# Performance work log

Measured on AMD Instinct MI355X. Metric: run time of the kernel, lower is better.

Reference implementation:

```python
import jax, jax.numpy as jnp
import numpy as np

EPS = 1e-5  # BatchNorm1d default eps


def _xavier_uniform(key, shape):
    # torch xavier: fan_in = shape[1]*prod(shape[2:]), fan_out = shape[0]*prod(shape[2:])
    rf = int(np.prod(shape[2:])) if len(shape) > 2 else 1
    fan_in = shape[1] * rf
    fan_out = shape[0] * rf
    bound = float(np.sqrt(6.0 / (fan_in + fan_out)))
    return jax.random.uniform(key, shape, jnp.float32, -bound, bound)


def setup_inputs() -> dict:
    key = jax.random.key(0)
    ks = jax.random.split(key, 6)
    d_in, h1, h2, d_out = 256, 512, 512, 256
    B = 4096
    x = jax.random.normal(ks[0], (B, 1, d_in), dtype=jnp.float32)
    W1 = _xavier_uniform(ks[1], (h1, d_in))
    b1 = jnp.zeros((h1,), jnp.float32)
    gamma = jnp.ones((1, 1, 1), jnp.float32)   # BatchNorm1d(1) weight
    beta = jnp.zeros((1, 1, 1), jnp.float32)   # BatchNorm1d(1) bias
    coeffs2 = _xavier_uniform(ks[2], (2, h2, h1, 16))
    bias2 = jnp.zeros((1, h2), jnp.float32)
    coeffs3 = _xavier_uniform(ks[3], (2, d_out, h2, 8))
    bias3 = jnp.zeros((1, d_out), jnp.float32)
    return {"x": x, "W1": W1, "b1": b1, "gamma": gamma, "beta": beta,
            "coeffs2": coeffs2, "bias2": bias2, "coeffs3": coeffs3, "bias3": bias3}


def _fourier_kan(x, coeffs, bias, gridsize):
    # x: (N, in)  coeffs: (2, out, in, grid)  ->  (N, out)
    k = jnp.arange(1, gridsize + 1, dtype=x.dtype)          # (grid,)
    arg = x[:, :, None] * k                                  # (N, in, grid) -- basis computed ONCE
    y = jnp.einsum('nig,oig->no', jnp.cos(arg), coeffs[0])
    y = y + jnp.einsum('nig,oig->no', jnp.sin(arg), coeffs[1])
    return y + bias


def reference(x, W1, b1, gamma, beta, coeffs2, bias2, coeffs3, bias3):
    # x: (B, 1, d_in)
    h = jnp.einsum('bcd,hd->bch', x, W1) + b1                # Linear -> (B,1,h1)
    # BatchNorm1d(1), training-mode batch stats over (N, L) for the single channel
    mean = jnp.mean(h, axis=(0, 2), keepdims=True)
    var = jnp.mean((h - mean) ** 2, axis=(0, 2), keepdims=True)
    h = gamma * (h - mean) * jax.lax.rsqrt(var + EPS) + beta
    h = jax.nn.relu(h)
    h = h.reshape(-1, h.shape[-1])                           # (B, h1)
    h = _fourier_kan(h, coeffs2, bias2, 16)                  # (B, h2)
    h = _fourier_kan(h, coeffs3, bias3, 8)                   # (B, out)
    return jax.nn.softmax(h, axis=1)
```

## Files before the change

kernel.cpp:

```cpp
#include <hip/hip_runtime.h>
#include <hip/hip_fp16.h>
#include <stdint.h>

typedef unsigned short u16;
typedef unsigned int u32;
typedef long i64;
typedef short bf16x8 __attribute__((ext_vector_type(8)));
typedef float f32x4 __attribute__((ext_vector_type(4)));

#define SCALE_C   1024.f
#define INV_SCALE 0.0009765625f

__device__ __forceinline__ float bf2f(u16 v) { return __uint_as_float(((u32)v) << 16); }

__device__ __forceinline__ u16 f2bf(float a) {
  u32 u = __float_as_uint(a); u += 0x7FFFu + ((u >> 16) & 1u); return (u16)(u >> 16);
}

__device__ __forceinline__ u32 packbf2(float a, float b) {
  u32 ua = __float_as_uint(a); ua += 0x7FFFu + ((ua >> 16) & 1u);
  u32 ub = __float_as_uint(b); ub += 0x7FFFu + ((ub >> 16) & 1u);
  return (ua >> 16) | (ub & 0xFFFF0000u);
}

__device__ __forceinline__ u32 packfp8x4(float a, float b, float c, float d) {
  u32 lo = (u32)__builtin_amdgcn_cvt_pk_fp8_f32(a, b, 0, false);
  return (u32)__builtin_amdgcn_cvt_pk_fp8_f32(c, d, (int)lo, true);
}

__device__ __forceinline__ float inval(const void* p, int idx, int isf) {
  return isf ? ((const float*)p)[idx] : bf2f(((const u16*)p)[idx]);
}

__device__ __forceinline__ void async_cp16(const void* g, void* l) {
  __builtin_amdgcn_global_load_lds(
      (const __attribute__((address_space(1))) void*)g,
      (__attribute__((address_space(3))) void*)l, 16, 0, 0);
}

__device__ __forceinline__ void basis16(float a, u32* pk) {
  float s1, c1; __sincosf(a, &s1, &c1);
  float t2 = c1 + c1;
  float cg[16], sg[16];
  cg[0] = c1; sg[0] = s1;
  cg[1] = fmaf(t2, c1, -1.f); sg[1] = t2 * s1;
  #pragma unroll
  for (int g = 2; g < 16; ++g) {
    cg[g] = fmaf(t2, cg[g-1], -cg[g-2]);
    sg[g] = fmaf(t2, sg[g-1], -sg[g-2]);
  }
  #pragma unroll
  for (int j = 0; j < 4; ++j) pk[j]   = packfp8x4(cg[4*j], cg[4*j+1], cg[4*j+2], cg[4*j+3]);
  #pragma unroll
  for (int j = 0; j < 4; ++j) pk[4+j] = packfp8x4(sg[4*j], sg[4*j+1], sg[4*j+2], sg[4*j+3]);
}

__device__ __forceinline__ void basis8(float a, u32* pk) {
  float s1, c1; __sincosf(a, &s1, &c1);
  float t2 = c1 + c1;
  float cg[8], sg[8];
  cg[0] = c1; sg[0] = s1;
  cg[1] = fmaf(t2, c1, -1.f); sg[1] = t2 * s1;
  #pragma unroll
  for (int g = 2; g < 8; ++g) {
    cg[g] = fmaf(t2, cg[g-1], -cg[g-2]);
    sg[g] = fmaf(t2, sg[g-1], -sg[g-2]);
  }
  pk[0] = packfp8x4(cg[0], cg[1], cg[2], cg[3]);
  pk[1] = packfp8x4(cg[4], cg[5], cg[6], cg[7]);
  pk[2] = packfp8x4(sg[0], sg[1], sg[2], sg[3]);
  pk[3] = packfp8x4(sg[4], sg[5], sg[6], sg[7]);
}

#define QOF(k) ((size_t)((k) < 6 ? (k) * 4 : 26 + ((k) - 6) * 4) << 20)

__device__ __forceinline__ void split_body(
    const void* __restrict__ src, u16* __restrict__ dst, int i, int isf, int lo_pos)
{
  int row = i >> 6, g = i & 63;
  float v[4];
  if (isf) {
    float4 t = ((const float4*)src)[i];
    v[0] = t.x; v[1] = t.y; v[2] = t.z; v[3] = t.w;
  } else {
    uint2 t = ((const uint2*)src)[i];
    const u16* p = (const u16*)&t;
    v[0] = bf2f(p[0]); v[1] = bf2f(p[1]); v[2] = bf2f(p[2]); v[3] = bf2f(p[3]);
  }
  u16 hi[4]; float lo[4];
  #pragma unroll
  for (int j = 0; j < 4; ++j) { hi[j] = f2bf(v[j]); lo[j] = v[j] - bf2f(hi[j]); }
  u32 hw0 = (u32)hi[0] | ((u32)hi[1] << 16);
  u32 hw1 = (u32)hi[2] | ((u32)hi[3] << 16);
  u32 lw0 = packbf2(lo[0], lo[1]);
  u32 lw1 = packbf2(lo[2], lo[3]);
  u32* base = (u32*)(dst + (size_t)row * 768);
  int c = g * 2;
  base[c] = hw0; base[c + 1] = hw1;
  if (lo_pos == 1) {
    base[128 + c] = lw0; base[128 + c + 1] = lw1;
    base[256 + c] = hw0; base[256 + c + 1] = hw1;
  } else {
    base[128 + c] = hw0; base[128 + c + 1] = hw1;
    base[256 + c] = lw0; base[256 + c + 1] = lw1;
  }
}

__global__ __launch_bounds__(256) void prep_all_kernel(
    const void* __restrict__ x, const void* __restrict__ W1,
    u16* __restrict__ Xs, u16* __restrict__ W1s,
    const void* __restrict__ c2, unsigned char* __restrict__ w2f8,
    const void* __restrict__ c3, unsigned char* __restrict__ w3f8,
    int* __restrict__ flag)
{
  __shared__ int sf[4];
  const int t = threadIdx.x, wave = t >> 6;
  {
    float v = fabsf(bf2f(((const u16*)W1)[t & 127]));
    int bad = !(v < 1e6f);
    unsigned long long b = __ballot(bad);
    if ((t & 63) == 0) sf[wave] = (b != 0ull) ? 1 : 0;
  }
  __syncthreads();
  const int isf = sf[0] | sf[1] | sf[2] | sf[3];
  const int bid = blockIdx.x;
  if (bid == 0 && t == 0) *flag = isf;
  if (bid < 1024) {
    split_body(x, Xs, bid * 256 + t, isf, 1);
  } else if (bid < 1152) {
    split_body(W1, W1s, (bid - 1024) * 256 + t, isf, 2);
  } else if (bid < 2176) {
    int u = (bid - 1152) * 256 + t;
    int o = u >> 9, i = u & 511;
    u32* d = (u32*)(w2f8 + (size_t)o * 16384 + i * 32);
    if (isf) {
      const float4* f0 = (const float4*)((const float*)c2 + ((size_t)o * 512 + i) * 16);
      const float4* f1 = (const float4*)((const float*)c2 + (size_t)512 * 512 * 16 + ((size_t)o * 512 + i) * 16);
      #pragma unroll
      for (int j = 0; j < 4; ++j) { float4 v = f0[j]; d[j]   = packfp8x4(v.x*SCALE_C, v.y*SCALE_C, v.z*SCALE_C, v.w*SCALE_C); }
      #pragma unroll
      for (int j = 0; j < 4; ++j) { float4 v = f1[j]; d[4+j] = packfp8x4(v.x*SCALE_C, v.y*SCALE_C, v.z*SCALE_C, v.w*SCALE_C); }
    } else {
      const u16* s0 = (const u16*)c2 + ((size_t)o * 512 + i) * 16;
      const u16* s1 = (const u16*)c2 + (size_t)512 * 512 * 16 + ((size_t)o * 512 + i) * 16;
      #pragma unroll
      for (int j = 0; j < 4; ++j) d[j]   = packfp8x4(bf2f(s0[4*j])*SCALE_C, bf2f(s0[4*j+1])*SCALE_C, bf2f(s0[4*j+2])*SCALE_C, bf2f(s0[4*j+3])*SCALE_C);
      #pragma unroll
      for (int j = 0; j < 4; ++j) d[4+j] = packfp8x4(bf2f(s1[4*j])*SCALE_C, bf2f(s1[4*j+1])*SCALE_C, bf2f(s1[4*j+2])*SCALE_C, bf2f(s1[4*j+3])*SCALE_C);
    }
  } else {
    int u = (bid - 2176) * 256 + t;
    int o = u >> 9, i = u & 511;
    u32* d = (u32*)(w3f8 + (size_t)o * 8192 + i * 16);
    if (isf) {
      const float4* f0 = (const float4*)((const float*)c3 + ((size_t)o * 512 + i) * 8);
      const float4* f1 = (const float4*)((const float*)c3 + (size_t)256 * 512 * 8 + ((size_t)o * 512 + i) * 8);
      #pragma unroll
      for (int j = 0; j < 2; ++j) { float4 v = f0[j]; d[j]   = packfp8x4(v.x*SCALE_C, v.y*SCALE_C, v.z*SCALE_C, v.w*SCALE_C); }
      #pragma unroll
      for (int j = 0; j < 2; ++j) { float4 v = f1[j]; d[2+j] = packfp8x4(v.x*SCALE_C, v.y*SCALE_C, v.z*SCALE_C, v.w*SCALE_C); }
    } else {
      const u16* s0 = (const u16*)c3 + ((size_t)o * 512 + i) * 8;
      const u16* s1 = (const u16*)c3 + (size_t)256 * 512 * 8 + ((size_t)o * 512 + i) * 8;
      #pragma unroll
      for (int j = 0; j < 2; ++j) d[j]   = packfp8x4(bf2f(s0[4*j])*SCALE_C, bf2f(s0[4*j+1])*SCALE_C, bf2f(s0[4*j+2])*SCALE_C, bf2f(s0[4*j+3])*SCALE_C);
      #pragma unroll
      for (int j = 0; j < 2; ++j) d[2+j] = packfp8x4(bf2f(s1[4*j])*SCALE_C, bf2f(s1[4*j+1])*SCALE_C, bf2f(s1[4*j+2])*SCALE_C, bf2f(s1[4*j+3])*SCALE_C);
    }
  }
}

#define L1_LD 136
__global__ __launch_bounds__(256) void l1_kernel(
    const u16* __restrict__ xs, const u16* __restrict__ w1s, const void* __restrict__ b1,
    const int* __restrict__ flag, float* __restrict__ H, float2* __restrict__ PT)
{
  __shared__ u16 sA[64 * L1_LD];
  __shared__ u16 sB[64 * L1_LD];
  __shared__ float redbuf[8];
  const int n0 = blockIdx.x * 64, o0 = blockIdx.y * 64;
  const int t = threadIdx.x, wave = t >> 6, lane = t & 63, quad = lane >> 4, l16 = lane & 15;
  const int isf = *flag;
  f32x4 acc[4] = {};
  for (int ks = 0; ks < 768; ks += 128) {
    #pragma unroll
    for (int r = 0; r < 4; ++r) {
      int idx = t + r * 256, row = idx >> 4, col = idx & 15;
      *(uint4*)&sA[row * L1_LD + col * 8] =
          *((const uint4*)(xs + (size_t)(n0 + row) * 768 + ks) + col);
    }
    #pragma unroll
    for (int r = 0; r < 4; ++r) {
      int idx = t + r * 256, row = idx >> 4, col = idx & 15;
      *(uint4*)&sB[row * L1_LD + col * 8] =
          *((const uint4*)(w1s + (size_t)(o0 + row) * 768 + ks) + col);
    }
    __syncthreads();
    #pragma unroll
    for (int kk = 0; kk < 128; kk += 32) {
      bf16x8 av = *(const bf16x8*)&sA[(wave * 16 + l16) * L1_LD + kk + quad * 8];
      #pragma unroll
      for (int fo = 0; fo < 4; ++fo) {
        bf16x8 bv = *(const bf16x8*)&sB[(fo * 16 + l16) * L1_LD + kk + quad * 8];
        acc[fo] = __builtin_amdgcn_mfma_f32_16x16x32_bf16(av, bv, acc[fo], 0, 0, 0);
      }
    }
    __syncthreads();
  }
  float s = 0.f, sq = 0.f;
  #pragma unroll
  for (int fo = 0; fo < 4; ++fo) {
    int o = o0 + fo * 16 + l16;
    float bias = inval(b1, o, isf);
    #pragma unroll
    for (int r = 0; r < 4; ++r) {
      int n = n0 + wave * 16 + quad * 4 + r;
      float h = acc[fo][r] + bias;
      H[(size_t)n * 512 + o] = h;
      s += h; sq += h * h;
    }
  }
  #pragma unroll
  for (int off = 32; off; off >>= 1) { s += __shfl_down(s, off); sq += __shfl_down(sq, off); }
  if (lane == 0) { redbuf[wave] = s; redbuf[4 + wave] = sq; }
  __syncthreads();
  if (t == 0) {
    float S = redbuf[0] + redbuf[1] + redbuf[2] + redbuf[3];
    float Q = redbuf[4] + redbuf[5] + redbuf[6] + redbuf[7];
    PT[blockIdx.y * 64 + blockIdx.x] = make_float2(S, Q);
  }
}

#define K2_LDB 128
__global__ __launch_bounds__(512, 4) void kan2_kernel(
    const float* __restrict__ H, const unsigned char* __restrict__ w2f8,
    const void* __restrict__ gammap, const void* __restrict__ betap,
    const int* __restrict__ flag, const float2* __restrict__ PT,
    float* __restrict__ P, int kzT)
{
  __shared__ __attribute__((aligned(16))) unsigned char smem[81920];
  float* sred = (float*)(smem + 81888);
  const int n0 = blockIdx.x * 64, o0 = blockIdx.y * 256, kz = blockIdx.z;
  const int t = threadIdx.x, wave = t >> 6, lane = t & 63, quad = lane >> 4, l16 = lane & 15;
  const int nst = 128 / kzT;
  const int i0 = kz * nst * 4;
  const int csw = (l16 & 7) << 4;
  const int isf = *flag;

  const int pt = t - 256;
  const int am = pt >> 2, ai = pt & 3;
  const int r0 = pt >> 3, seg = pt & 7;
  const unsigned char* bsrc = w2f8 + (size_t)(o0 + (r0 & 63)) * 16384 + (size_t)i0 * 32
                              + (((seg & 7) * 16) ^ ((r0 & 7) << 4));
  const float* hsrc = H + (size_t)(n0 + (am & 63)) * 512 + i0 + (ai & 3);
  const int acol0 = ((ai & 3) * 32) ^ ((am & 7) << 4);
  const int acol1 = ((ai & 3) * 32 + 16) ^ ((am & 7) << 4);
  float mean = 0.f, gs = 0.f, beta = 0.f, ph = 0.f;
  u32 pk[8];

  if (wave >= 4) {
    unsigned char* b0 = smem + 16384 + (wave - 4) * 1024;
    #pragma unroll
    for (int p = 0; p < 8; ++p)
      async_cp16(bsrc + (size_t)p * 32 * 16384, b0 + p * 4096);
    float2 pa = PT[pt], pb = PT[pt + 256];
    float ss = pa.x + pb.x, qs = pa.y + pb.y;
    #pragma unroll
    for (int off = 32; off; off >>= 1) { ss += __shfl_down(ss, off); qs += __shfl_down(qs, off); }
    if (lane == 0) { sred[(wave - 4) * 2] = ss; sred[(wave - 4) * 2 + 1] = qs; }
  }
  __syncthreads();
  if (wave >= 4) {
    const float Ssum = sred[0] + sred[2] + sred[4] + sred[6];
    const float Qsum = sred[1] + sred[3] + sred[5] + sred[7];
    const float Nn = 4096.f * 512.f;
    mean = Ssum / Nn;
    const float rstd = rsqrtf(Qsum / Nn - mean * mean + 1e-5f);
    gs = inval(gammap, 0, isf) * rstd;
    beta = inval(betap, 0, isf);
    float a = fmaxf((*hsrc - mean) * gs + beta, 0.f);
    hsrc += 4;
    basis16(a, pk);
    *(uint4*)&smem[am * K2_LDB + acol0] = *(uint4*)&pk[0];
    *(uint4*)&smem[am * K2_LDB + acol1] = *(uint4*)&pk[4];
    if (nst > 1) { ph = *hsrc; hsrc += 4; }
  }
  __syncthreads();

  f32x4 acc[2][8] = {};
  const int wm = (wave & 1) * 32, wo = (wave >> 1) * 128;
  int cur = 0;
  for (int s = 0; s < nst; ++s) {
    const int nxt = cur ^ 1;
    if (wave >= 4) {
      if (s + 1 < nst) {
        bsrc += 128;
        unsigned char* bn = smem + 16384 + nxt * 32768 + (wave - 4) * 1024;
        #pragma unroll
        for (int p = 0; p < 8; ++p)
          async_cp16(bsrc + (size_t)p * 32 * 16384, bn + p * 4096);
        float a = fmaxf((ph - mean) * gs + beta, 0.f);
        basis16(a, pk);
        unsigned char* an = smem + nxt * 8192;
        *(uint4*)&an[am * K2_LDB + acol0] = *(uint4*)&pk[0];
        *(uint4*)&an[am * K2_LDB + acol1] = *(uint4*)&pk[4];
        if (s + 2 < nst) { ph = *hsrc; hsrc += 4; }
      }
    } else {
      const unsigned char* ac = smem + cur * 8192;
      const unsigned char* bc = smem + 16384 + cur * 32768;
      #pragma unroll
      for (int kk = 0; kk < 128; kk += 32) {
        const int cb = (kk + quad * 8) ^ csw;
        i64 bfr[8], afr[2];
        #pragma unroll
        for (int fo = 0; fo < 8; ++fo)
          bfr[fo] = *(const i64*)&bc[(wo + fo * 16 + l16) * K2_LDB + cb];
        #pragma unroll
        for (int fm = 0; fm < 2; ++fm)
          afr[fm] = *(const i64*)&ac[(wm + fm * 16 + l16) * K2_LDB + cb];
        #pragma unroll
        for (int fm = 0; fm < 2; ++fm)
        #pragma unroll
        for (int fo = 0; fo < 8; ++fo)
          acc[fm][fo] = __builtin_amdgcn_mfma_f32_16x16x32_fp8_fp8(afr[fm], bfr[fo], acc[fm][fo], 0, 0, 0);
      }
    }
    __syncthreads();
    cur = nxt;
  }
  if (wave < 4) {
    float* Pk = P + (size_t)kz * (4096 * 512);
    #pragma unroll
    for (int fm = 0; fm < 2; ++fm)
    #pragma unroll
    for (int fo = 0; fo < 8; ++fo) {
      int o = o0 + wo + fo * 16 + l16;
      #pragma unroll
      for (int r = 0; r < 4; ++r) {
        int n = n0 + wm + fm * 16 + quad * 4 + r;
        Pk[(size_t)n * 512 + o] = acc[fm][fo][r] * INV_SCALE;
      }
    }
  }
}

#define K3_LDB 128
__global__ __launch_bounds__(512, 4) void kan3_kernel(
    const float* __restrict__ P2, const void* __restrict__ bias2,
    const unsigned char* __restrict__ w3f8,
    const int* __restrict__ flag, char* __restrict__ wsbase, int kzT2)
{
  __shared__ __attribute__((aligned(16))) unsigned char smem[81920];
  const int n0 = blockIdx.x * 64, kz = blockIdx.z;
  const int t = threadIdx.x, wave = t >> 6, lane = t & 63, quad = lane >> 4, l16 = lane & 15;
  const int i0 = kz * 64;
  const int nst = 8;
  const int csw = (l16 & 7) << 4;
  const int isf = *flag;

  const int pt = t - 256;
  const int am = (pt >> 2) & 63;
  const int il = (pt & 3) * 2;
  const int r0 = (pt >> 3) & 31, seg = pt & 7;
  const unsigned char* bsrc = w3f8 + (size_t)r0 * 8192 + (size_t)i0 * 16
                              + ((seg * 16) ^ ((r0 & 7) << 4));
  const float* psrc = P2 + (size_t)(n0 + am) * 512 + i0 + il;
  const int acol0 = (il * 16) ^ ((am & 7) << 4);
  const int acol1 = ((il + 1) * 16) ^ ((am & 7) << 4);
  float2 ph2 = make_float2(0.f, 0.f);
  u32 pkA[4], pkB[4];

  if (wave >= 4) {
    unsigned char* b0 = smem + 16384 + (wave - 4) * 1024;
    #pragma unroll
    for (int p = 0; p < 8; ++p)
      async_cp16(bsrc + (size_t)p * 32 * 8192, b0 + p * 4096);
    float v0 = inval(bias2, i0 + il, isf);
    float v1 = inval(bias2, i0 + il + 1, isf);
    for (int k = 0; k < kzT2; ++k) {
      float2 pp = *(const float2*)(psrc + (size_t)k * 4096 * 512);
      v0 += pp.x; v1 += pp.y;
    }
    basis8(v0, pkA); basis8(v1, pkB);
    *(uint4*)&smem[am * K3_LDB + acol0] = *(uint4*)&pkA[0];
    *(uint4*)&smem[am * K3_LDB + acol1] = *(uint4*)&pkB[0];
    psrc += 8;
    float w0 = inval(bias2, i0 + 8 + il, isf);
    float w1 = inval(bias2, i0 + 8 + il + 1, isf);
    for (int k = 0; k < kzT2; ++k) {
      float2 pp = *(const float2*)(psrc + (size_t)k * 4096 * 512);
      w0 += pp.x; w1 += pp.y;
    }
    ph2 = make_float2(w0, w1);
  }
  __syncthreads();

  f32x4 acc[4][4] = {};
  const int wo = wave * 64;
  int cur = 0;
  for (int s = 0; s < nst; ++s) {
    const int nxt = cur ^ 1;
    if (wave >= 4) {
      if (s + 1 < nst) {
        bsrc += 128;
        unsigned char* bn = smem + 16384 + nxt * 32768 + (wave - 4) * 1024;
        #pragma unroll
        for (int p = 0; p < 8; ++p)
          async_cp16(bsrc + (size_t)p * 32 * 8192, bn + p * 4096);
        basis8(ph2.x, pkA); basis8(ph2.y, pkB);
        unsigned char* an = smem + nxt * 8192;
        *(uint4*)&an[am * K3_LDB + acol0] = *(uint4*)&pkA[0];
        *(uint4*)&an[am * K3_LDB + acol1] = *(uint4*)&pkB[0];
        if (s + 2 < nst) {
          psrc += 8;
          float w0 = inval(bias2, i0 + (s + 2) * 8 + il, isf);
          float w1 = inval(bias2, i0 + (s + 2) * 8 + il + 1, isf);
          for (int k = 0; k < kzT2; ++k) {
            float2 pp = *(const float2*)(psrc + (size_t)k * 4096 * 512);
            w0 += pp.x; w1 += pp.y;
          }
          ph2 = make_float2(w0, w1);
        }
      }
    } else {
      const unsigned char* ac = smem + cur * 8192;
      const unsigned char* bc = smem + 16384 + cur * 32768;
      __builtin_amdgcn_s_setprio(1);
      #pragma unroll
      for (int kk = 0; kk < 128; kk += 32) {
        const int cb = (kk + quad * 8) ^ csw;
        i64 bfr[4], afr[4];
        #pragma unroll
        for (int fo = 0; fo < 4; ++fo)
          bfr[fo] = *(const i64*)&bc[(wo + fo * 16 + l16) * K3_LDB + cb];
        #pragma unroll
        for (int fm = 0; fm < 4; ++fm)
          afr[fm] = *(const i64*)&ac[(fm * 16 + l16) * K3_LDB + cb];
        #pragma unroll
        for (int fm = 0; fm < 4; ++fm)
        #pragma unroll
        for (int fo = 0; fo < 4; ++fo)
          acc[fm][fo] = __builtin_amdgcn_mfma_f32_16x16x32_fp8_fp8(afr[fm], bfr[fo], acc[fm][fo], 0, 0, 0);
      }
      __builtin_amdgcn_s_setprio(0);
    }
    __syncthreads();
    cur = nxt;
  }
  if (wave < 4) {
    float* Qk = (float*)(wsbase + QOF(kz));
    #pragma unroll
    for (int fm = 0; fm < 4; ++fm)
    #pragma unroll
    for (int fo = 0; fo < 4; ++fo) {
      int o = wo + fo * 16 + l16;
      #pragma unroll
      for (int r = 0; r < 4; ++r) {
        int n = n0 + fm * 16 + quad * 4 + r;
        Qk[(size_t)n * 256 + o] = acc[fm][fo][r] * INV_SCALE;
      }
    }
  }
}

__global__ __launch_bounds__(256) void softmax_kernel(
    const char* __restrict__ wsbase, const void* __restrict__ bias3,
    const int* __restrict__ flag, float* __restrict__ out)
{
  const int t = threadIdx.x, wave = t >> 6, lane = t & 63;
  const int row = blockIdx.x * 4 + wave;
  const int isf = *flag;
  size_t base = (size_t)row * 256 + lane * 4;
  float v0 = 0.f, v1 = 0.f, v2 = 0.f, v3 = 0.f;
  #pragma unroll
  for (int k = 0; k < 8; ++k) {
    float4 a = *(const float4*)((const float*)(wsbase + QOF(k)) + base);
    v0 += a.x; v1 += a.y; v2 += a.z; v3 += a.w;
  }
  int o = lane * 4;
  v0 += inval(bias3, o + 0, isf);
  v1 += inval(bias3, o + 1, isf);
  v2 += inval(bias3, o + 2, isf);
  v3 += inval(bias3, o + 3, isf);
  float m = fmaxf(fmaxf(v0, v1), fmaxf(v2, v3));
  #pragma unroll
  for (int off = 32; off; off >>= 1) m = fmaxf(m, __shfl_xor(m, off));
  float e0 = __expf(v0 - m), e1 = __expf(v1 - m), e2 = __expf(v2 - m), e3 = __expf(v3 - m);
  float s = e0 + e1 + e2 + e3;
  #pragma unroll
  for (int off = 32; off; off >>= 1) s += __shfl_xor(s, off);
  float inv = 1.f / s;
  *(float4*)(out + base) = make_float4(e0 * inv, e1 * inv, e2 * inv, e3 * inv);
}

extern "C" void kernel_launch(void* const* d_in, const int* in_sizes, int n_in,
                              void* d_out, int out_size, void* d_ws, size_t ws_size,
                              hipStream_t stream)
{
  const void* x     = d_in[0];
  const void* W1    = d_in[1];
  const void* b1    = d_in[2];
  const void* gamma = d_in[3];
  const void* beta  = d_in[4];
  const void* c2    = d_in[5];
  const void* bias2 = d_in[6];
  const void* c3    = d_in[7];
  const void* bias3 = d_in[8];

  const int kz2 = 4;

  char* ws = (char*)d_ws;
  float*          H    = (float*)(ws + 0);
  unsigned char*  W2F8 = (unsigned char*)(ws + (16ull << 20));
  unsigned char*  W3F8 = (unsigned char*)(ws + (24ull << 20));
  u16*            Xs   = (u16*)(ws + (26ull << 20));
  u16*            W1s  = (u16*)(ws + (33ull << 20));
  float*          P2   = (float*)(ws + (34ull << 20));
  size_t tail = (34ull << 20) + (size_t)kz2 * (8ull << 20) + 524288;
  float2* PT   = (float2*)(ws + tail);
  int*    FLAG = (int*)   (ws + tail + 65536);

  prep_all_kernel<<<dim3(2688), dim3(256), 0, stream>>>(x, W1, Xs, W1s, c2, W2F8, c3, W3F8, FLAG);
  l1_kernel   <<<dim3(64, 8), dim3(256), 0, stream>>>(Xs, W1s, b1, FLAG, H, PT);
  kan2_kernel <<<dim3(64, 2, kz2), dim3(512), 0, stream>>>(H, W2F8, gamma, beta, FLAG, PT, P2, kz2);
  kan3_kernel <<<dim3(64, 1, 8), dim3(512), 0, stream>>>(P2, bias2, W3F8, FLAG, ws, kz2);
  softmax_kernel<<<dim3(1024), dim3(256), 0, stream>>>(ws, bias3, FLAG, (float*)d_out);
}
```

Baseline: 195.2 us.

## Replace split-K partial buffers with atomic accumulation into zeroed buffers

Split-K partial sums in the two KAN layers are now accumulated with float atomics into one buffer per layer, instead of being written as separate slices and summed by the consumer kernels. The prep kernel gets extra blocks that zero the accumulation buffers (12MB). This cuts the consumer-side reads of 4 or 8 partial slices and shrinks the workspace footprint. In exchange it adds atomic traffic and a zeroing pass, and makes the summation order nondeterministic.

```diff
diff --git a/kernel.cpp b/kernel.cpp
--- a/kernel.cpp
+++ b/kernel.cpp
@@ -36,6 +36,10 @@
   __builtin_amdgcn_global_load_lds(
       (const __attribute__((address_space(1))) void*)g,
       (__attribute__((address_space(3))) void*)l, 16, 0, 0);
+}
+
+__device__ __forceinline__ void atomic_fadd(float* p, float v) {
+  (void)unsafeAtomicAdd(p, v);
 }
 
 __device__ __forceinline__ void basis16(float a, u32* pk) {
@@ -71,8 +75,6 @@
   pk[2] = packfp8x4(sg[0], sg[1], sg[2], sg[3]);
   pk[3] = packfp8x4(sg[4], sg[5], sg[6], sg[7]);
 }
-
-#define QOF(k) ((size_t)((k) < 6 ? (k) * 4 : 26 + ((k) - 6) * 4) << 20)
 
 __device__ __forceinline__ void split_body(
     const void* __restrict__ src, u16* __restrict__ dst, int i, int isf, int lo_pos)
@@ -111,10 +113,18 @@
     u16* __restrict__ Xs, u16* __restrict__ W1s,
     const void* __restrict__ c2, unsigned char* __restrict__ w2f8,
     const void* __restrict__ c3, unsigned char* __restrict__ w3f8,
-    int* __restrict__ flag)
+    int* __restrict__ flag, unsigned char* __restrict__ zero_base)
 {
   __shared__ int sf[4];
   const int t = threadIdx.x, wave = t >> 6;
+  const int bid = blockIdx.x;
+  if (bid >= 2688) {
+    uint4* dst = (uint4*)(zero_base + (size_t)(bid - 2688) * 65536);
+    uint4 z = make_uint4(0, 0, 0, 0);
+    #pragma unroll
+    for (int j = 0; j < 16; ++j) dst[j * 256 + t] = z;
+    return;
+  }
   {
     float v = fabsf(bf2f(((const u16*)W1)[t & 127]));
     int bad = !(v < 1e6f);
@@ -123,7 +133,6 @@
   }
   __syncthreads();
   const int isf = sf[0] | sf[1] | sf[2] | sf[3];
-  const int bid = blockIdx.x;
   if (bid == 0 && t == 0) *flag = isf;
   if (bid < 1024) {
     split_body(x, Xs, bid * 256 + t, isf, 1);
@@ -330,7 +339,6 @@
     cur = nxt;
   }
   if (wave < 4) {
-    float* Pk = P + (size_t)kz * (4096 * 512);
     #pragma unroll
     for (int fm = 0; fm < 2; ++fm)
     #pragma unroll
@@ -339,7 +347,7 @@
       #pragma unroll
       for (int r = 0; r < 4; ++r) {
         int n = n0 + wm + fm * 16 + quad * 4 + r;
-        Pk[(size_t)n * 512 + o] = acc[fm][fo][r] * INV_SCALE;
+        atomic_fadd(&P[(size_t)n * 512 + o], acc[fm][fo][r] * INV_SCALE);
       }
     }
   }
@@ -349,7 +357,7 @@
 __global__ __launch_bounds__(512, 4) void kan3_kernel(
     const float* __restrict__ P2, const void* __restrict__ bias2,
     const unsigned char* __restrict__ w3f8,
-    const int* __restrict__ flag, char* __restrict__ wsbase, int kzT2)
+    const int* __restrict__ flag, float* __restrict__ Q3)
 {
   __shared__ __attribute__((aligned(16))) unsigned char smem[81920];
   const int n0 = blockIdx.x * 64, kz = blockIdx.z;
@@ -376,23 +384,16 @@
     #pragma unroll
     for (int p = 0; p < 8; ++p)
       async_cp16(bsrc + (size_t)p * 32 * 8192, b0 + p * 4096);
-    float v0 = inval(bias2, i0 + il, isf);
-    float v1 = inval(bias2, i0 + il + 1, isf);
-    for (int k = 0; k < kzT2; ++k) {
-      float2 pp = *(const float2*)(psrc + (size_t)k * 4096 * 512);
-      v0 += pp.x; v1 += pp.y;
-    }
+    float2 pp = *(const float2*)psrc;
+    float v0 = inval(bias2, i0 + il, isf) + pp.x;
+    float v1 = inval(bias2, i0 + il + 1, isf) + pp.y;
     basis8(v0, pkA); basis8(v1, pkB);
     *(uint4*)&smem[am * K3_LDB + acol0] = *(uint4*)&pkA[0];
     *(uint4*)&smem[am * K3_LDB + acol1] = *(uint4*)&pkB[0];
     psrc += 8;
-    float w0 = inval(bias2, i0 + 8 + il, isf);
-    float w1 = inval(bias2, i0 + 8 + il + 1, isf);
-    for (int k = 0; k < kzT2; ++k) {
-      float2 pp = *(const float2*)(psrc + (size_t)k * 4096 * 512);
-      w0 += pp.x; w1 += pp.y;
-    }
-    ph2 = make_float2(w0, w1);
+    float2 pq = *(const float2*)psrc;
+    ph2 = make_float2(inval(bias2, i0 + 8 + il, isf) + pq.x,
+                      inval(bias2, i0 + 8 + il + 1, isf) + pq.y);
   }
   __syncthreads();
 
@@ -414,13 +415,9 @@
         *(uint4*)&an[am * K3_LDB + acol1] = *(uint4*)&pkB[0];
         if (s + 2 < nst) {
           psrc += 8;
-          float w0 = inval(bias2, i0 + (s + 2) * 8 + il, isf);
-          float w1 = inval(bias2, i0 + (s + 2) * 8 + il + 1, isf);
-          for (int k = 0; k < kzT2; ++k) {
-            float2 pp = *(const float2*)(psrc + (size_t)k * 4096 * 512);
-            w0 += pp.x; w1 += pp.y;
-          }
-          ph2 = make_float2(w0, w1);
+          float2 pq = *(const float2*)psrc;
+          ph2 = make_float2(inval(bias2, i0 + (s + 2) * 8 + il, isf) + pq.x,
+                            inval(bias2, i0 + (s + 2) * 8 + il + 1, isf) + pq.y);
         }
       }
     } else {
@@ -449,7 +446,6 @@
     cur = nxt;
   }
   if (wave < 4) {
-    float* Qk = (float*)(wsbase + QOF(kz));
     #pragma unroll
     for (int fm = 0; fm < 4; ++fm)
     #pragma unroll
@@ -458,31 +454,26 @@
       #pragma unroll
       for (int r = 0; r < 4; ++r) {
         int n = n0 + fm * 16 + quad * 4 + r;
-        Qk[(size_t)n * 256 + o] = acc[fm][fo][r] * INV_SCALE;
+        atomic_fadd(&Q3[(size_t)n * 256 + o], acc[fm][fo][r] * INV_SCALE);
       }
     }
   }
 }
 
 __global__ __launch_bounds__(256) void softmax_kernel(
-    const char* __restrict__ wsbase, const void* __restrict__ bias3,
+    const float* __restrict__ Q, const void* __restrict__ bias3,
     const int* __restrict__ flag, float* __restrict__ out)
 {
   const int t = threadIdx.x, wave = t >> 6, lane = t & 63;
   const int row = blockIdx.x * 4 + wave;
   const int isf = *flag;
   size_t base = (size_t)row * 256 + lane * 4;
-  float v0 = 0.f, v1 = 0.f, v2 = 0.f, v3 = 0.f;
-  #pragma unroll
-  for (int k = 0; k < 8; ++k) {
-    float4 a = *(const float4*)((const float*)(wsbase + QOF(k)) + base);
-    v0 += a.x; v1 += a.y; v2 += a.z; v3 += a.w;
-  }
+  float4 a = *(const float4*)(Q + base);
   int o = lane * 4;
-  v0 += inval(bias3, o + 0, isf);
-  v1 += inval(bias3, o + 1, isf);
-  v2 += inval(bias3, o + 2, isf);
-  v3 += inval(bias3, o + 3, isf);
+  float v0 = a.x + inval(bias3, o + 0, isf);
+  float v1 = a.y + inval(bias3, o + 1, isf);
+  float v2 = a.z + inval(bias3, o + 2, isf);
+  float v3 = a.w + inval(bias3, o + 3, isf);
   float m = fmaxf(fmaxf(v0, v1), fmaxf(v2, v3));
   #pragma unroll
   for (int off = 32; off; off >>= 1) m = fmaxf(m, __shfl_xor(m, off));
@@ -511,19 +502,20 @@
   const int kz2 = 4;
 
   char* ws = (char*)d_ws;
-  float*          H    = (float*)(ws + 0);
-  unsigned char*  W2F8 = (unsigned char*)(ws + (16ull << 20));
-  unsigned char*  W3F8 = (unsigned char*)(ws + (24ull << 20));
-  u16*            Xs   = (u16*)(ws + (26ull << 20));
-  u16*            W1s  = (u16*)(ws + (33ull << 20));
-  float*          P2   = (float*)(ws + (34ull << 20));
-  size_t tail = (34ull << 20) + (size_t)kz2 * (8ull << 20) + 524288;
-  float2* PT   = (float2*)(ws + tail);
-  int*    FLAG = (int*)   (ws + tail + 65536);
-
-  prep_all_kernel<<<dim3(2688), dim3(256), 0, stream>>>(x, W1, Xs, W1s, c2, W2F8, c3, W3F8, FLAG);
+  float*          H     = (float*)(ws + 0);
+  unsigned char*  W2F8  = (unsigned char*)(ws + (16ull << 20));
+  unsigned char*  W3F8  = (unsigned char*)(ws + (24ull << 20));
+  u16*            Xs    = (u16*)(ws + (26ull << 20));
+  u16*            W1s   = (u16*)(ws + (33ull << 20));
+  float*          P2ACC = (float*)(ws + (34ull << 20));
+  float*          Q3ACC = (float*)(ws + (42ull << 20));
+  float2*         PT    = (float2*)(ws + (47ull << 20));
+  int*            FLAG  = (int*)  (ws + (47ull << 20) + 65536);
+  unsigned char*  ZBASE = (unsigned char*)(ws + (34ull << 20));
+
+  prep_all_kernel<<<dim3(2880), dim3(256), 0, stream>>>(x, W1, Xs, W1s, c2, W2F8, c3, W3F8, FLAG, ZBASE);
   l1_kernel   <<<dim3(64, 8), dim3(256), 0, stream>>>(Xs, W1s, b1, FLAG, H, PT);
-  kan2_kernel <<<dim3(64, 2, kz2), dim3(512), 0, stream>>>(H, W2F8, gamma, beta, FLAG, PT, P2, kz2);
-  kan3_kernel <<<dim3(64, 1, 8), dim3(512), 0, stream>>>(P2, bias2, W3F8, FLAG, ws, kz2);
-  softmax_kernel<<<dim3(1024), dim3(256), 0, stream>>>(ws, bias3, FLAG, (float*)d_out);
-}
+  kan2_kernel <<<dim3(64, 2, kz2), dim3(512), 0, stream>>>(H, W2F8, gamma, beta, FLAG, PT, P2ACC, kz2);
+  kan3_kernel <<<dim3(64, 1, 8), dim3(512), 0, stream>>>(P2ACC, bias2, W3F8, FLAG, Q3ACC);
+  softmax_kernel<<<dim3(1024), dim3(256), 0, stream>>>(Q3ACC, bias3, FLAG, (float*)d_out);
+}
```

Result: slower. 245.0 us (+25.5%).

## Drop split-K in kan3, tile over rows and outputs with full-K loop

Applied to the files above, without the earlier changes.

Replaces kan3's 8-way split-K grid (64x1x8, 64 rows by 256 outputs per block) with a 128x2 grid of 32 rows by 128 outputs, each block looping over the full K in 32 stages. This removes the eight partial-sum buffers and the 8-way reduction in softmax, which now reads a single Q3 buffer. The cost is fewer MFMAs per shared-memory A load and more serial stages per block. Each block still recomputes the fourier basis for its rows across the whole input dimension, doubled across the two output tiles.

```diff
diff --git a/kernel.cpp b/kernel.cpp
--- a/kernel.cpp
+++ b/kernel.cpp
@@ -71,8 +71,6 @@
   pk[2] = packfp8x4(sg[0], sg[1], sg[2], sg[3]);
   pk[3] = packfp8x4(sg[4], sg[5], sg[6], sg[7]);
 }
-
-#define QOF(k) ((size_t)((k) < 6 ? (k) * 4 : 26 + ((k) - 6) * 4) << 20)
 
 __device__ __forceinline__ void split_body(
     const void* __restrict__ src, u16* __restrict__ dst, int i, int isf, int lo_pos)
@@ -345,49 +343,49 @@
   }
 }
 
-#define K3_LDB 128
+#define K3_ROW 256
 __global__ __launch_bounds__(512, 4) void kan3_kernel(
     const float* __restrict__ P2, const void* __restrict__ bias2,
     const unsigned char* __restrict__ w3f8,
-    const int* __restrict__ flag, char* __restrict__ wsbase, int kzT2)
+    const int* __restrict__ flag, float* __restrict__ Q3, int kzT2)
 {
   __shared__ __attribute__((aligned(16))) unsigned char smem[81920];
-  const int n0 = blockIdx.x * 64, kz = blockIdx.z;
+  const int n0 = blockIdx.x * 32, o0 = blockIdx.y * 128;
   const int t = threadIdx.x, wave = t >> 6, lane = t & 63, quad = lane >> 4, l16 = lane & 15;
-  const int i0 = kz * 64;
-  const int nst = 8;
+  const int nst = 32;
   const int csw = (l16 & 7) << 4;
   const int isf = *flag;
 
   const int pt = t - 256;
-  const int am = (pt >> 2) & 63;
-  const int il = (pt & 3) * 2;
-  const int r0 = (pt >> 3) & 31, seg = pt & 7;
-  const unsigned char* bsrc = w3f8 + (size_t)r0 * 8192 + (size_t)i0 * 16
-                              + ((seg * 16) ^ ((r0 & 7) << 4));
-  const float* psrc = P2 + (size_t)(n0 + am) * 512 + i0 + il;
+  const int am = (pt >> 3) & 31;
+  const int il = (pt & 7) * 2;
+  const int brow0 = ((pt >> 6) & 3) * 4 + ((pt & 63) >> 4);
+  const int bcol = (pt & 15) * 16;
+  const int scol = bcol ^ ((brow0 & 7) << 4);
+  const unsigned char* bsrc = w3f8 + (size_t)(o0 + brow0) * 8192 + scol;
+  const float* psrc = P2 + (size_t)(n0 + am) * 512 + il;
   const int acol0 = (il * 16) ^ ((am & 7) << 4);
   const int acol1 = ((il + 1) * 16) ^ ((am & 7) << 4);
   float2 ph2 = make_float2(0.f, 0.f);
   u32 pkA[4], pkB[4];
 
   if (wave >= 4) {
-    unsigned char* b0 = smem + 16384 + (wave - 4) * 1024;
-    #pragma unroll
-    for (int p = 0; p < 8; ++p)
-      async_cp16(bsrc + (size_t)p * 32 * 8192, b0 + p * 4096);
-    float v0 = inval(bias2, i0 + il, isf);
-    float v1 = inval(bias2, i0 + il + 1, isf);
+    unsigned char* b0 = smem + 16384 + (pt >> 6) * 1024;
+    #pragma unroll
+    for (int q = 0; q < 8; ++q)
+      async_cp16(bsrc + (size_t)q * 16 * 8192, b0 + q * 4096);
+    float v0 = inval(bias2, il, isf);
+    float v1 = inval(bias2, il + 1, isf);
     for (int k = 0; k < kzT2; ++k) {
       float2 pp = *(const float2*)(psrc + (size_t)k * 4096 * 512);
       v0 += pp.x; v1 += pp.y;
     }
     basis8(v0, pkA); basis8(v1, pkB);
-    *(uint4*)&smem[am * K3_LDB + acol0] = *(uint4*)&pkA[0];
-    *(uint4*)&smem[am * K3_LDB + acol1] = *(uint4*)&pkB[0];
-    psrc += 8;
-    float w0 = inval(bias2, i0 + 8 + il, isf);
-    float w1 = inval(bias2, i0 + 8 + il + 1, isf);
+    *(uint4*)&smem[am * K3_ROW + acol0] = *(uint4*)&pkA[0];
+    *(uint4*)&smem[am * K3_ROW + acol1] = *(uint4*)&pkB[0];
+    psrc += 16;
+    float w0 = inval(bias2, 16 + il, isf);
+    float w1 = inval(bias2, 16 + il + 1, isf);
     for (int k = 0; k < kzT2; ++k) {
       float2 pp = *(const float2*)(psrc + (size_t)k * 4096 * 512);
       w0 += pp.x; w1 += pp.y;
@@ -396,26 +394,26 @@
   }
   __syncthreads();
 
-  f32x4 acc[4][4] = {};
-  const int wo = wave * 64;
+  f32x4 acc[4] = {};
+  const int wm = (wave & 1) * 16, wo = (wave >> 1) * 64;
   int cur = 0;
   for (int s = 0; s < nst; ++s) {
     const int nxt = cur ^ 1;
     if (wave >= 4) {
       if (s + 1 < nst) {
-        bsrc += 128;
-        unsigned char* bn = smem + 16384 + nxt * 32768 + (wave - 4) * 1024;
-        #pragma unroll
-        for (int p = 0; p < 8; ++p)
-          async_cp16(bsrc + (size_t)p * 32 * 8192, bn + p * 4096);
+        bsrc += 256;
+        unsigned char* bn = smem + 16384 + nxt * 32768 + (pt >> 6) * 1024;
+        #pragma unroll
+        for (int q = 0; q < 8; ++q)
+          async_cp16(bsrc + (size_t)q * 16 * 8192, bn + q * 4096);
         basis8(ph2.x, pkA); basis8(ph2.y, pkB);
         unsigned char* an = smem + nxt * 8192;
-        *(uint4*)&an[am * K3_LDB + acol0] = *(uint4*)&pkA[0];
-        *(uint4*)&an[am * K3_LDB + acol1] = *(uint4*)&pkB[0];
+        *(uint4*)&an[am * K3_ROW + acol0] = *(uint4*)&pkA[0];
+        *(uint4*)&an[am * K3_ROW + acol1] = *(uint4*)&pkB[0];
         if (s + 2 < nst) {
-          psrc += 8;
-          float w0 = inval(bias2, i0 + (s + 2) * 8 + il, isf);
-          float w1 = inval(bias2, i0 + (s + 2) * 8 + il + 1, isf);
+          psrc += 16;
+          float w0 = inval(bias2, (s + 2) * 16 + il, isf);
+          float w1 = inval(bias2, (s + 2) * 16 + il + 1, isf);
           for (int k = 0; k < kzT2; ++k) {
             float2 pp = *(const float2*)(psrc + (size_t)k * 4096 * 512);
             w0 += pp.x; w1 += pp.y;
@@ -428,20 +426,16 @@
       const unsigned char* bc = smem + 16384 + cur * 32768;
       __builtin_amdgcn_s_setprio(1);
       #pragma unroll
-      for (int kk = 0; kk < 128; kk += 32) {
+      for (int kk = 0; kk < 256; kk += 32) {
         const int cb = (kk + quad * 8) ^ csw;
-        i64 bfr[4], afr[4];
+        i64 bfr[4];
         #pragma unroll
         for (int fo = 0; fo < 4; ++fo)
-          bfr[fo] = *(const i64*)&bc[(wo + fo * 16 + l16) * K3_LDB + cb];
-        #pragma unroll
-        for (int fm = 0; fm < 4; ++fm)
-          afr[fm] = *(const i64*)&ac[(fm * 16 + l16) * K3_LDB + cb];
-        #pragma unroll
-        for (int fm = 0; fm < 4; ++fm)
+          bfr[fo] = *(const i64*)&bc[(wo + fo * 16 + l16) * K3_ROW + cb];
+        i64 af = *(const i64*)&ac[(wm + l16) * K3_ROW + cb];
         #pragma unroll
         for (int fo = 0; fo < 4; ++fo)
-          acc[fm][fo] = __builtin_amdgcn_mfma_f32_16x16x32_fp8_fp8(afr[fm], bfr[fo], acc[fm][fo], 0, 0, 0);
+          acc[fo] = __builtin_amdgcn_mfma_f32_16x16x32_fp8_fp8(af, bfr[fo], acc[fo], 0, 0, 0);
       }
       __builtin_amdgcn_s_setprio(0);
     }
@@ -449,40 +443,32 @@
     cur = nxt;
   }
   if (wave < 4) {
-    float* Qk = (float*)(wsbase + QOF(kz));
-    #pragma unroll
-    for (int fm = 0; fm < 4; ++fm)
     #pragma unroll
     for (int fo = 0; fo < 4; ++fo) {
-      int o = wo + fo * 16 + l16;
+      int o = o0 + wo + fo * 16 + l16;
       #pragma unroll
       for (int r = 0; r < 4; ++r) {
-        int n = n0 + fm * 16 + quad * 4 + r;
-        Qk[(size_t)n * 256 + o] = acc[fm][fo][r] * INV_SCALE;
+        int n = n0 + wm + quad * 4 + r;
+        Q3[(size_t)n * 256 + o] = acc[fo][r] * INV_SCALE;
       }
     }
   }
 }
 
 __global__ __launch_bounds__(256) void softmax_kernel(
-    const char* __restrict__ wsbase, const void* __restrict__ bias3,
+    const float* __restrict__ Q, const void* __restrict__ bias3,
     const int* __restrict__ flag, float* __restrict__ out)
 {
   const int t = threadIdx.x, wave = t >> 6, lane = t & 63;
   const int row = blockIdx.x * 4 + wave;
   const int isf = *flag;
   size_t base = (size_t)row * 256 + lane * 4;
-  float v0 = 0.f, v1 = 0.f, v2 = 0.f, v3 = 0.f;
-  #pragma unroll
-  for (int k = 0; k < 8; ++k) {
-    float4 a = *(const float4*)((const float*)(wsbase + QOF(k)) + base);
-    v0 += a.x; v1 += a.y; v2 += a.z; v3 += a.w;
-  }
+  float4 a = *(const float4*)(Q + base);
   int o = lane * 4;
-  v0 += inval(bias3, o + 0, isf);
-  v1 += inval(bias3, o + 1, isf);
-  v2 += inval(bias3, o + 2, isf);
-  v3 += inval(bias3, o + 3, isf);
+  float v0 = a.x + inval(bias3, o + 0, isf);
+  float v1 = a.y + inval(bias3, o + 1, isf);
+  float v2 = a.z + inval(bias3, o + 2, isf);
+  float v3 = a.w + inval(bias3, o + 3, isf);
   float m = fmaxf(fmaxf(v0, v1), fmaxf(v2, v3));
   #pragma unroll
   for (int off = 32; off; off >>= 1) m = fmaxf(m, __shfl_xor(m, off));
@@ -517,6 +503,7 @@
   u16*            Xs   = (u16*)(ws + (26ull << 20));
   u16*            W1s  = (u16*)(ws + (33ull << 20));
   float*          P2   = (float*)(ws + (34ull << 20));
+  float*          Q3   = (float*)(ws + 0);
   size_t tail = (34ull << 20) + (size_t)kz2 * (8ull << 20) + 524288;
   float2* PT   = (float2*)(ws + tail);
   int*    FLAG = (int*)   (ws + tail + 65536);
@@ -524,6 +511,6 @@
   prep_all_kernel<<<dim3(2688), dim3(256), 0, stream>>>(x, W1, Xs, W1s, c2, W2F8, c3, W3F8, FLAG);
   l1_kernel   <<<dim3(64, 8), dim3(256), 0, stream>>>(Xs, W1s, b1, FLAG, H, PT);
   kan2_kernel <<<dim3(64, 2, kz2), dim3(512), 0, stream>>>(H, W2F8, gamma, beta, FLAG, PT, P2, kz2);
-  kan3_kernel <<<dim3(64, 1, 8), dim3(512), 0, stream>>>(P2, bias2, W3F8, FLAG, ws, kz2);
-  softmax_kernel<<<dim3(1024), dim3(256), 0, stream>>>(ws, bias3, FLAG, (float*)d_out);
-}
+  kan3_kernel <<<dim3(128, 2), dim3(512), 0, stream>>>(P2, bias2, W3F8, FLAG, Q3, kz2);
+  softmax_kernel<<<dim3(1024), dim3(256), 0, stream>>>(Q3, bias3, FLAG, (float*)d_out);
+}
```

Measured after the change: 223.6 us. 14.6% more time.

## Double-buffer layer-1 GEMM tiles with async global-to-LDS copies and XOR swizzle

Applied to the files above, without the earlier changes.

Replaces the synchronous register-staged tile loads in l1_kernel with async 16-byte global-to-LDS copies into two 32KB buffers. The next K-slice is prefetched while the MFMAs run on the current one, leaving one barrier per step. The padded LDS layout is replaced by an XOR swizzle to avoid bank conflicts. LDS use grows to 64KB per block, which may reduce occupancy, and correctness depends on async_cp16 completing before the barrier.

```diff
diff --git a/kernel.cpp b/kernel.cpp
--- a/kernel.cpp
+++ b/kernel.cpp
@@ -170,42 +170,56 @@
   }
 }
 
-#define L1_LD 136
 __global__ __launch_bounds__(256) void l1_kernel(
     const u16* __restrict__ xs, const u16* __restrict__ w1s, const void* __restrict__ b1,
     const int* __restrict__ flag, float* __restrict__ H, float2* __restrict__ PT)
 {
-  __shared__ u16 sA[64 * L1_LD];
-  __shared__ u16 sB[64 * L1_LD];
+  __shared__ __attribute__((aligned(16))) unsigned char smem[65536];
   __shared__ float redbuf[8];
   const int n0 = blockIdx.x * 64, o0 = blockIdx.y * 64;
   const int t = threadIdx.x, wave = t >> 6, lane = t & 63, quad = lane >> 4, l16 = lane & 15;
   const int isf = *flag;
+  const int srow = lane >> 4;
+  const int scol = (lane & 15) * 16;
   f32x4 acc[4] = {};
-  for (int ks = 0; ks < 768; ks += 128) {
-    #pragma unroll
-    for (int r = 0; r < 4; ++r) {
-      int idx = t + r * 256, row = idx >> 4, col = idx & 15;
-      *(uint4*)&sA[row * L1_LD + col * 8] =
-          *((const uint4*)(xs + (size_t)(n0 + row) * 768 + ks) + col);
-    }
-    #pragma unroll
-    for (int r = 0; r < 4; ++r) {
-      int idx = t + r * 256, row = idx >> 4, col = idx & 15;
-      *(uint4*)&sB[row * L1_LD + col * 8] =
-          *((const uint4*)(w1s + (size_t)(o0 + row) * 768 + ks) + col);
-    }
+  #pragma unroll
+  for (int p = 0; p < 4; ++p) {
+    int row = (wave * 4 + p) * 4 + srow;
+    int sb = scol ^ ((row & 7) << 4);
+    async_cp16(xs  + (size_t)(n0 + row) * 768 + (sb >> 1),
+               smem + (wave * 4 + p) * 1024);
+    async_cp16(w1s + (size_t)(o0 + row) * 768 + (sb >> 1),
+               smem + 16384 + (wave * 4 + p) * 1024);
+  }
+  int cur = 0;
+  for (int s = 0; s < 6; ++s) {
     __syncthreads();
+    if (s + 1 < 6) {
+      const int ksn = (s + 1) * 128;
+      unsigned char* bufn = smem + (cur ^ 1) * 32768;
+      #pragma unroll
+      for (int p = 0; p < 4; ++p) {
+        int row = (wave * 4 + p) * 4 + srow;
+        int sb = scol ^ ((row & 7) << 4);
+        async_cp16(xs  + (size_t)(n0 + row) * 768 + ksn + (sb >> 1),
+                   bufn + (wave * 4 + p) * 1024);
+        async_cp16(w1s + (size_t)(o0 + row) * 768 + ksn + (sb >> 1),
+                   bufn + 16384 + (wave * 4 + p) * 1024);
+      }
+    }
+    const unsigned char* ba = smem + cur * 32768;
+    const unsigned char* bb = ba + 16384;
     #pragma unroll
     for (int kk = 0; kk < 128; kk += 32) {
-      bf16x8 av = *(const bf16x8*)&sA[(wave * 16 + l16) * L1_LD + kk + quad * 8];
+      const int cb = (kk * 2 + quad * 16) ^ ((l16 & 7) << 4);
+      bf16x8 av = *(const bf16x8*)&ba[(wave * 16 + l16) * 256 + cb];
       #pragma unroll
       for (int fo = 0; fo < 4; ++fo) {
-        bf16x8 bv = *(const bf16x8*)&sB[(fo * 16 + l16) * L1_LD + kk + quad * 8];
+        bf16x8 bv = *(const bf16x8*)&bb[(fo * 16 + l16) * 256 + cb];
         acc[fo] = __builtin_amdgcn_mfma_f32_16x16x32_bf16(av, bv, acc[fo], 0, 0, 0);
       }
     }
-    __syncthreads();
+    cur ^= 1;
   }
   float s = 0.f, sq = 0.f;
   #pragma unroll
```

After: 193.4 us. About the same (-0.9%).
